# Performance work log

Measured on AMD Instinct MI355X. Metric: run time of the kernel, lower is better.

The kernel has to match this reference:

```python
import jax, jax.numpy as jnp
import numpy as np

EMBED_DIMS = 192
NUM_HEADS = 6
WH, WW = 7, 7
N_TOK = WH * WW
B_WIN = 4096


def _rpe_index(Wh, Ww):
    coords = np.array([[x, y] for x in range(Ww) for y in range(Wh)])  # [N,2]
    d = coords[None, :, :] - coords[:, None, :]                        # [N,N,2]
    idx = (d[:, :, 0] + Ww - 1) * (2 * Ww - 1) + (d[:, :, 1] + Wh - 1)
    return idx.T  # transpose(0,1) as in the torch code


def setup_inputs() -> dict:
    key = jax.random.key(0)
    ks = jax.random.split(key, 6)
    C = EMBED_DIMS
    return {
        "x": jax.random.normal(ks[0], (B_WIN, N_TOK, C), dtype=jnp.float32),
        "qkv_w": jax.random.normal(ks[1], (3 * C, C), dtype=jnp.float32) * 0.02,
        "qkv_b": jax.random.normal(ks[2], (3 * C,), dtype=jnp.float32) * 0.02,
        "proj_w": jax.random.normal(ks[3], (C, C), dtype=jnp.float32) * 0.02,
        "proj_b": jax.random.normal(ks[4], (C,), dtype=jnp.float32) * 0.02,
        "rpe_table": jax.random.normal(ks[5], ((2 * WH - 1) * (2 * WW - 1), NUM_HEADS), dtype=jnp.float32),
        "rpe_idx": jnp.asarray(_rpe_index(WH, WW), dtype=jnp.int32),
    }


def reference(x, qkv_w, qkv_b, proj_w, proj_b, rpe_table, rpe_idx):
    B, N, C = x.shape
    H = NUM_HEADS
    hd = C // H
    scale = hd ** -0.5
    # qkv projection: torch Linear is x @ W.T + b
    qkv = x @ qkv_w.T + qkv_b                      # [B, N, 3C]
    qkv = qkv.reshape(B, N, 3, H, hd).transpose(2, 0, 3, 1, 4)  # [3, B, H, N, hd]
    q, k, v = qkv[0] * scale, qkv[1], qkv[2]
    attn = jnp.einsum("bhnd,bhmd->bhnm", q, k)     # [B, H, N, N]
    # relative position bias gather: table[idx] -> [N, N, H] -> [H, N, N]
    bias = rpe_table[rpe_idx].transpose(2, 0, 1)
    attn = jax.nn.softmax(attn + bias, axis=-1)
    out = jnp.einsum("bhnm,bhmd->bhnd", attn, v)   # [B, H, N, hd]
    out = out.transpose(0, 2, 1, 3).reshape(B, N, C)
    return out @ proj_w.T + proj_b
```

## Files before the change

kernel.cpp:

```cpp
#include <hip/hip_runtime.h>
#include <stdint.h>

#define NWIN 4096
#define NTOK 49
#define CDIM 192
#define NH   6
#define HD   32

typedef __attribute__((ext_vector_type(8))) short short8;
typedef __attribute__((ext_vector_type(4))) float floatx4;
typedef unsigned short ushort_t;
typedef unsigned int uint32;

#define XS_S 200
#define QK_S 136
#define P_S  72
#define VT_S 72

#define OFF_XS   0
#define OFF_QKS  9800
#define OFF_PB   16464
#define OFF_VT   19992
#define LDS_TOT  24600

__device__ __forceinline__ ushort_t f2bf(float f) {
    uint32 u = __float_as_uint(f);
    u += 0x7fffu + ((u >> 16) & 1u);
    return (ushort_t)(u >> 16);
}

__global__ void wmsa_prologue(const float* __restrict__ qkv_w,
                              const float* __restrict__ proj_w,
                              const float* __restrict__ rpe_table,
                              const int*   __restrict__ rpe_idx,
                              ushort_t* __restrict__ qkv_wb,
                              ushort_t* __restrict__ proj_wb,
                              float* __restrict__ biasws)
{
    int i = blockIdx.x * 256 + threadIdx.x;
    if (i < 110592) {
        qkv_wb[i] = f2bf(qkv_w[i]);
    } else if (i < 147456) {
        proj_wb[i - 110592] = f2bf(proj_w[i - 110592]);
    } else if (i < 147456 + NH * NTOK * 64) {
        int r = i - 147456;
        int h = r / (NTOK * 64);
        int rem = r - h * (NTOK * 64);
        int n = rem >> 6, m = rem & 63;
        biasws[r] = (m < NTOK) ? rpe_table[rpe_idx[n * NTOK + m] * NH + h] : 0.f;
    }
}

__global__ __launch_bounds__(256)
void wmsa_mfma(const float* __restrict__ x,
               const ushort_t* __restrict__ qkv_wb,
               const float* __restrict__ qkv_b,
               const ushort_t* __restrict__ proj_wb,
               const float* __restrict__ proj_b,
               const float* __restrict__ biasws,
               float* __restrict__ out)
{
    __shared__ alignas(16) ushort_t lds[LDS_TOT];
    ushort_t* const xs  = lds + OFF_XS;
    ushort_t* const qks = lds + OFF_QKS;
    ushort_t* const Pb  = lds + OFF_PB;
    ushort_t* const Vt  = lds + OFF_VT;

    const int b    = blockIdx.x;
    const int t    = threadIdx.x;
    const int w    = t >> 6;
    const int lane = t & 63;
    const int quad = lane >> 4;
    const int c    = lane & 15;
    const float scale = 0.17677669529663687f;

    const float* xb = x + (size_t)b * (NTOK * CDIM);

    for (int i = t; i < (NTOK * CDIM) / 4; i += 256) {
        int e = i * 4;
        int n = e / CDIM, d = e - n * CDIM;
        float4 v = *(const float4*)(xb + e);
        ushort_t* p = &xs[n * XS_S + d];
        p[0] = f2bf(v.x); p[1] = f2bf(v.y); p[2] = f2bf(v.z); p[3] = f2bf(v.w);
    }
    __syncthreads();

    floatx4 out_acc[NH][2];
    const floatx4 zf = {0.f, 0.f, 0.f, 0.f};
    #pragma unroll
    for (int h = 0; h < NH; ++h) { out_acc[h][0] = zf; out_acc[h][1] = zf; }

    const int hh_w   = w >> 1;
    const int half_w = w & 1;
    const int jcol   = hh_w * 64 + half_w * 16 + c;

    #pragma unroll
    for (int pass = 0; pass < 3; ++pass) {
        const int jbase = (2 * pass + hh_w) * HD + half_w * 16 + c;
        floatx4 acc[3][4];
        #pragma unroll
        for (int s = 0; s < 3; ++s)
            #pragma unroll
            for (int mt = 0; mt < 4; ++mt) acc[s][mt] = zf;

        #pragma unroll
        for (int ks = 0; ks < 6; ++ks) {
            short8 a4[4];
            #pragma unroll
            for (int mt = 0; mt < 4; ++mt)
                a4[mt] = *(const short8*)&xs[(mt * 16 + c) * XS_S + ks * 32 + quad * 8];
            #pragma unroll
            for (int s = 0; s < 3; ++s) {
                short8 bf = *(const short8*)&qkv_wb[(s * CDIM + jbase) * CDIM + ks * 32 + quad * 8];
                #pragma unroll
                for (int mt = 0; mt < 4; ++mt)
                    acc[s][mt] = __builtin_amdgcn_mfma_f32_16x16x32_bf16(
                        a4[mt], bf, acc[s][mt], 0, 0, 0);
            }
        }
        float bq = qkv_b[jbase];
        float bk = qkv_b[CDIM + jbase];
        float bv = qkv_b[2 * CDIM + jbase];
        #pragma unroll
        for (int mt = 0; mt < 4; ++mt) {
            #pragma unroll
            for (int r = 0; r < 4; ++r) {
                int n = mt * 16 + quad * 4 + r;
                if (n < NTOK) {
                    qks[n * QK_S + jcol]      = f2bf((acc[0][mt][r] + bq) * scale);
                    qks[n * QK_S + jcol + 32] = f2bf(acc[1][mt][r] + bk);
                }
                Vt[(w * 16 + c) * VT_S + n] =
                    (n < NTOK) ? f2bf(acc[2][mt][r] + bv) : (ushort_t)0;
            }
        }
        __syncthreads();

        #pragma unroll
        for (int hh = 0; hh < 2; ++hh) {
            const int h = pass * 2 + hh;

            short8 aq = *(const short8*)&qks[(w * 16 + c) * QK_S + hh * 64 + quad * 8];
            floatx4 sacc[4];
            #pragma unroll
            for (int nt = 0; nt < 4; ++nt) {
                short8 bk8 = *(const short8*)&qks[(nt * 16 + c) * QK_S + hh * 64 + 32 + quad * 8];
                sacc[nt] = __builtin_amdgcn_mfma_f32_16x16x32_bf16(aq, bk8, zf, 0, 0, 0);
            }

            const float* bpb = biasws + h * (NTOK * 64);
            #pragma unroll
            for (int r = 0; r < 4; ++r) {
                int n  = w * 16 + quad * 4 + r;
                int nc = (n < NTOK) ? n : (NTOK - 1);
                float sv[4];
                #pragma unroll
                for (int nt = 0; nt < 4; ++nt) {
                    int col = nt * 16 + c;
                    float bias = bpb[nc * 64 + col];
                    sv[nt] = (col < NTOK) ? (sacc[nt][r] + bias) : -1e30f;
                }
                float m0 = fmaxf(fmaxf(sv[0], sv[1]), fmaxf(sv[2], sv[3]));
                m0 = fmaxf(m0, __shfl_xor(m0, 1));
                m0 = fmaxf(m0, __shfl_xor(m0, 2));
                m0 = fmaxf(m0, __shfl_xor(m0, 4));
                m0 = fmaxf(m0, __shfl_xor(m0, 8));
                float ex[4], s0 = 0.f;
                #pragma unroll
                for (int nt = 0; nt < 4; ++nt) { ex[nt] = __expf(sv[nt] - m0); s0 += ex[nt]; }
                s0 += __shfl_xor(s0, 1);
                s0 += __shfl_xor(s0, 2);
                s0 += __shfl_xor(s0, 4);
                s0 += __shfl_xor(s0, 8);
                float inv = 1.f / s0;
                if (n < NTOK) {
                    #pragma unroll
                    for (int nt = 0; nt < 4; ++nt)
                        Pb[n * P_S + nt * 16 + c] = f2bf(ex[nt] * inv);
                }
            }

            #pragma unroll
            for (int ks2 = 0; ks2 < 2; ++ks2) {
                short8 ap = *(const short8*)&Pb[(w * 16 + c) * P_S + ks2 * 32 + quad * 8];
                #pragma unroll
                for (int nt = 0; nt < 2; ++nt) {
                    short8 bv8 = *(const short8*)&Vt[(hh * HD + nt * 16 + c) * VT_S + ks2 * 32 + quad * 8];
                    out_acc[h][nt] = __builtin_amdgcn_mfma_f32_16x16x32_bf16(
                        ap, bv8, out_acc[h][nt], 0, 0, 0);
                }
            }
        }
        if (pass < 2) __syncthreads();
    }

    #pragma unroll
    for (int h = 0; h < NH; ++h)
        #pragma unroll
        for (int nt = 0; nt < 2; ++nt)
            #pragma unroll
            for (int r = 0; r < 4; ++r) {
                int n = w * 16 + quad * 4 + r;
                if (n < NTOK)
                    xs[n * XS_S + h * HD + nt * 16 + c] = f2bf(out_acc[h][nt][r]);
            }
    __syncthreads();

    floatx4 pacc[3][4];
    #pragma unroll
    for (int tt = 0; tt < 3; ++tt)
        #pragma unroll
        for (int mt = 0; mt < 4; ++mt) pacc[tt][mt] = zf;

    #pragma unroll
    for (int ks = 0; ks < 6; ++ks) {
        short8 a4[4];
        #pragma unroll
        for (int mt = 0; mt < 4; ++mt)
            a4[mt] = *(const short8*)&xs[(mt * 16 + c) * XS_S + ks * 32 + quad * 8];
        #pragma unroll
        for (int tt = 0; tt < 3; ++tt) {
            int j = (tt * 4 + w) * 16 + c;
            short8 bf = *(const short8*)&proj_wb[j * CDIM + ks * 32 + quad * 8];
            #pragma unroll
            for (int mt = 0; mt < 4; ++mt)
                pacc[tt][mt] = __builtin_amdgcn_mfma_f32_16x16x32_bf16(
                    a4[mt], bf, pacc[tt][mt], 0, 0, 0);
        }
    }
    #pragma unroll
    for (int tt = 0; tt < 3; ++tt) {
        int j = (tt * 4 + w) * 16 + c;
        float pb = proj_b[j];
        #pragma unroll
        for (int mt = 0; mt < 4; ++mt)
            #pragma unroll
            for (int r = 0; r < 4; ++r) {
                int n = mt * 16 + quad * 4 + r;
                if (n < NTOK)
                    out[((size_t)b * NTOK + n) * CDIM + j] = pacc[tt][mt][r] + pb;
            }
    }
}

extern "C" void kernel_launch(void* const* d_in, const int* in_sizes, int n_in,
                              void* d_out, int out_size, void* d_ws, size_t ws_size,
                              hipStream_t stream)
{
    const float* x      = (const float*)d_in[0];
    const float* qkv_w  = (const float*)d_in[1];
    const float* qkv_b  = (const float*)d_in[2];
    const float* proj_w = (const float*)d_in[3];
    const float* proj_b = (const float*)d_in[4];
    const float* rpe_t  = (const float*)d_in[5];
    const int*   rpe_i  = (const int*)d_in[6];
    float*       o      = (float*)d_out;

    ushort_t* qkv_wb  = (ushort_t*)d_ws;
    ushort_t* proj_wb = qkv_wb + 110592;
    float*    biasws  = (float*)((char*)d_ws + (110592 + 36864) * sizeof(ushort_t));

    int tot = 147456 + NH * NTOK * 64;
    wmsa_prologue<<<dim3((tot + 255) / 256), dim3(256), 0, stream>>>(
        qkv_w, proj_w, rpe_t, rpe_i, qkv_wb, proj_wb, biasws);
    wmsa_mfma<<<dim3(NWIN), dim3(256), 0, stream>>>(
        x, qkv_wb, qkv_b, proj_wb, proj_b, biasws, o);
}
```

Baseline: 593.7 us.

## Repartition MMA work so each wave owns a 16-row token tile

Each wave now owns one 16-token row block across all matmuls instead of splitting output columns across waves. It keeps its x fragments in registers for the whole QKV stage and writes per-head attention outputs straight into LDS, which drops the 48 out_acc accumulators and one barrier. It also adds launch_bounds(256,3) to cut register pressure and raise occupancy. The cost is that each wave now reloads every QKV and projection weight fragment from global memory/L2 on its own, instead of reusing one B fragment across four M tiles, so weight traffic per block grows.

```diff
diff --git a/kernel.cpp b/kernel.cpp
--- a/kernel.cpp
+++ b/kernel.cpp
@@ -51,7 +51,7 @@
     }
 }
 
-__global__ __launch_bounds__(256)
+__global__ __launch_bounds__(256, 3)
 void wmsa_mfma(const float* __restrict__ x,
                const ushort_t* __restrict__ qkv_wb,
                const float* __restrict__ qkv_b,
@@ -73,6 +73,7 @@
     const int quad = lane >> 4;
     const int c    = lane & 15;
     const float scale = 0.17677669529663687f;
+    const floatx4 zf = {0.f, 0.f, 0.f, 0.f};
 
     const float* xb = x + (size_t)b * (NTOK * CDIM);
 
@@ -85,53 +86,48 @@
     }
     __syncthreads();
 
-    floatx4 out_acc[NH][2];
-    const floatx4 zf = {0.f, 0.f, 0.f, 0.f};
+    const int arow = w * 16 + c;
+    short8 af[6];
     #pragma unroll
-    for (int h = 0; h < NH; ++h) { out_acc[h][0] = zf; out_acc[h][1] = zf; }
-
-    const int hh_w   = w >> 1;
-    const int half_w = w & 1;
-    const int jcol   = hh_w * 64 + half_w * 16 + c;
-
-    #pragma unroll
+    for (int ks = 0; ks < 6; ++ks)
+        af[ks] = *(const short8*)&xs[arow * XS_S + ks * 32 + quad * 8];
+
     for (int pass = 0; pass < 3; ++pass) {
-        const int jbase = (2 * pass + hh_w) * HD + half_w * 16 + c;
-        floatx4 acc[3][4];
-        #pragma unroll
-        for (int s = 0; s < 3; ++s)
-            #pragma unroll
-            for (int mt = 0; mt < 4; ++mt) acc[s][mt] = zf;
-
-        #pragma unroll
-        for (int ks = 0; ks < 6; ++ks) {
-            short8 a4[4];
-            #pragma unroll
-            for (int mt = 0; mt < 4; ++mt)
-                a4[mt] = *(const short8*)&xs[(mt * 16 + c) * XS_S + ks * 32 + quad * 8];
-            #pragma unroll
-            for (int s = 0; s < 3; ++s) {
-                short8 bf = *(const short8*)&qkv_wb[(s * CDIM + jbase) * CDIM + ks * 32 + quad * 8];
+        #pragma unroll
+        for (int tg = 0; tg < 4; ++tg) {
+            const int hh   = tg >> 1;
+            const int half = tg & 1;
+            const int jb   = (2 * pass + hh) * HD + half * 16 + c;
+            const ushort_t* wp0 = qkv_wb + jb * CDIM + quad * 8;
+
+            floatx4 acc[3];
+            #pragma unroll
+            for (int s = 0; s < 3; ++s) acc[s] = zf;
+
+            #pragma unroll
+            for (int ks = 0; ks < 6; ++ks) {
                 #pragma unroll
-                for (int mt = 0; mt < 4; ++mt)
-                    acc[s][mt] = __builtin_amdgcn_mfma_f32_16x16x32_bf16(
-                        a4[mt], bf, acc[s][mt], 0, 0, 0);
-            }
-        }
-        float bq = qkv_b[jbase];
-        float bk = qkv_b[CDIM + jbase];
-        float bv = qkv_b[2 * CDIM + jbase];
-        #pragma unroll
-        for (int mt = 0; mt < 4; ++mt) {
-            #pragma unroll
-            for (int r = 0; r < 4; ++r) {
-                int n = mt * 16 + quad * 4 + r;
+                for (int s = 0; s < 3; ++s) {
+                    short8 bf = *(const short8*)(wp0 + s * (CDIM * CDIM) + ks * 32);
+                    acc[s] = __builtin_amdgcn_mfma_f32_16x16x32_bf16(
+                        af[ks], bf, acc[s], 0, 0, 0);
+                }
+            }
+
+            float bq = qkv_b[jb];
+            float bk = qkv_b[CDIM + jb];
+            float bv = qkv_b[2 * CDIM + jb];
+            const int qcol = hh * 64 + half * 16 + c;
+            const int vrow = hh * HD + half * 16 + c;
+            #pragma unroll
+            for (int r = 0; r < 4; ++r) {
+                int n = w * 16 + quad * 4 + r;
                 if (n < NTOK) {
-                    qks[n * QK_S + jcol]      = f2bf((acc[0][mt][r] + bq) * scale);
-                    qks[n * QK_S + jcol + 32] = f2bf(acc[1][mt][r] + bk);
-                }
-                Vt[(w * 16 + c) * VT_S + n] =
-                    (n < NTOK) ? f2bf(acc[2][mt][r] + bv) : (ushort_t)0;
+                    qks[n * QK_S + qcol]      = f2bf((acc[0][r] + bq) * scale);
+                    qks[n * QK_S + qcol + 32] = f2bf(acc[1][r] + bk);
+                }
+                Vt[vrow * VT_S + n] = (n < NTOK) ? f2bf(acc[2][r] + bv)
+                                                 : (ushort_t)0;
             }
         }
         __syncthreads();
@@ -140,7 +136,7 @@
         for (int hh = 0; hh < 2; ++hh) {
             const int h = pass * 2 + hh;
 
-            short8 aq = *(const short8*)&qks[(w * 16 + c) * QK_S + hh * 64 + quad * 8];
+            short8 aq = *(const short8*)&qks[arow * QK_S + hh * 64 + quad * 8];
             floatx4 sacc[4];
             #pragma unroll
             for (int nt = 0; nt < 4; ++nt) {
@@ -180,66 +176,59 @@
                 }
             }
 
+            floatx4 o0 = zf, o1 = zf;
             #pragma unroll
             for (int ks2 = 0; ks2 < 2; ++ks2) {
-                short8 ap = *(const short8*)&Pb[(w * 16 + c) * P_S + ks2 * 32 + quad * 8];
-                #pragma unroll
-                for (int nt = 0; nt < 2; ++nt) {
-                    short8 bv8 = *(const short8*)&Vt[(hh * HD + nt * 16 + c) * VT_S + ks2 * 32 + quad * 8];
-                    out_acc[h][nt] = __builtin_amdgcn_mfma_f32_16x16x32_bf16(
-                        ap, bv8, out_acc[h][nt], 0, 0, 0);
+                short8 ap  = *(const short8*)&Pb[arow * P_S + ks2 * 32 + quad * 8];
+                short8 bv0 = *(const short8*)&Vt[(hh * HD + c) * VT_S + ks2 * 32 + quad * 8];
+                short8 bv1 = *(const short8*)&Vt[(hh * HD + 16 + c) * VT_S + ks2 * 32 + quad * 8];
+                o0 = __builtin_amdgcn_mfma_f32_16x16x32_bf16(ap, bv0, o0, 0, 0, 0);
+                o1 = __builtin_amdgcn_mfma_f32_16x16x32_bf16(ap, bv1, o1, 0, 0, 0);
+            }
+            #pragma unroll
+            for (int r = 0; r < 4; ++r) {
+                int n = w * 16 + quad * 4 + r;
+                if (n < NTOK) {
+                    xs[n * XS_S + h * HD + c]      = f2bf(o0[r]);
+                    xs[n * XS_S + h * HD + 16 + c] = f2bf(o1[r]);
                 }
             }
         }
         if (pass < 2) __syncthreads();
     }
 
+    short8 ap6[6];
     #pragma unroll
-    for (int h = 0; h < NH; ++h)
-        #pragma unroll
-        for (int nt = 0; nt < 2; ++nt)
+    for (int ks = 0; ks < 6; ++ks)
+        ap6[ks] = *(const short8*)&xs[arow * XS_S + ks * 32 + quad * 8];
+
+    #pragma unroll
+    for (int tg = 0; tg < 4; ++tg) {
+        floatx4 pacc[3];
+        #pragma unroll
+        for (int tt = 0; tt < 3; ++tt) pacc[tt] = zf;
+
+        #pragma unroll
+        for (int ks = 0; ks < 6; ++ks) {
+            #pragma unroll
+            for (int tt = 0; tt < 3; ++tt) {
+                int j = (tg * 3 + tt) * 16 + c;
+                short8 bf = *(const short8*)&proj_wb[j * CDIM + ks * 32 + quad * 8];
+                pacc[tt] = __builtin_amdgcn_mfma_f32_16x16x32_bf16(
+                    ap6[ks], bf, pacc[tt], 0, 0, 0);
+            }
+        }
+        #pragma unroll
+        for (int tt = 0; tt < 3; ++tt) {
+            int j = (tg * 3 + tt) * 16 + c;
+            float pb = proj_b[j];
             #pragma unroll
             for (int r = 0; r < 4; ++r) {
                 int n = w * 16 + quad * 4 + r;
                 if (n < NTOK)
-                    xs[n * XS_S + h * HD + nt * 16 + c] = f2bf(out_acc[h][nt][r]);
-            }
-    __syncthreads();
-
-    floatx4 pacc[3][4];
-    #pragma unroll
-    for (int tt = 0; tt < 3; ++tt)
-        #pragma unroll
-        for (int mt = 0; mt < 4; ++mt) pacc[tt][mt] = zf;
-
-    #pragma unroll
-    for (int ks = 0; ks < 6; ++ks) {
-        short8 a4[4];
-        #pragma unroll
-        for (int mt = 0; mt < 4; ++mt)
-            a4[mt] = *(const short8*)&xs[(mt * 16 + c) * XS_S + ks * 32 + quad * 8];
-        #pragma unroll
-        for (int tt = 0; tt < 3; ++tt) {
-            int j = (tt * 4 + w) * 16 + c;
-            short8 bf = *(const short8*)&proj_wb[j * CDIM + ks * 32 + quad * 8];
-            #pragma unroll
-            for (int mt = 0; mt < 4; ++mt)
-                pacc[tt][mt] = __builtin_amdgcn_mfma_f32_16x16x32_bf16(
-                    a4[mt], bf, pacc[tt][mt], 0, 0, 0);
-        }
-    }
-    #pragma unroll
-    for (int tt = 0; tt < 3; ++tt) {
-        int j = (tt * 4 + w) * 16 + c;
-        float pb = proj_b[j];
-        #pragma unroll
-        for (int mt = 0; mt < 4; ++mt)
-            #pragma unroll
-            for (int r = 0; r < 4; ++r) {
-                int n = mt * 16 + quad * 4 + r;
-                if (n < NTOK)
-                    out[((size_t)b * NTOK + n) * CDIM + j] = pacc[tt][mt][r] + pb;
-            }
+                    out[((size_t)b * NTOK + n) * CDIM + j] = pacc[tt][r] + pb;
+            }
+        }
     }
 }
 
```

Result: slower. 940.5 us (+58.4%).

## Pack per-head attention outputs to bf16 registers and raise occupancy bound

Applied to the files above, without the earlier changes.

Replaces the 12 fp32 accumulator vectors held across all passes with per-head temporary accumulators that are packed into bf16 pairs, and writes the first four heads into xs before the last pass once xs is no longer needed. Adds a min-blocks-per-SM hint of 3 to launch_bounds. The aim is to cut register pressure so more workgroups fit per CU. The price is extra packing and unpacking instructions, and possible spills if the compiler is forced under the tighter register limit.

```diff
diff --git a/kernel.cpp b/kernel.cpp
--- a/kernel.cpp
+++ b/kernel.cpp
@@ -27,6 +27,9 @@
     uint32 u = __float_as_uint(f);
     u += 0x7fffu + ((u >> 16) & 1u);
     return (ushort_t)(u >> 16);
+}
+__device__ __forceinline__ uint32 pk2(float lo, float hi) {
+    return (uint32)f2bf(lo) | ((uint32)f2bf(hi) << 16);
 }
 
 __global__ void wmsa_prologue(const float* __restrict__ qkv_w,
@@ -51,7 +54,7 @@
     }
 }
 
-__global__ __launch_bounds__(256)
+__global__ __launch_bounds__(256, 3)
 void wmsa_mfma(const float* __restrict__ x,
                const ushort_t* __restrict__ qkv_wb,
                const float* __restrict__ qkv_b,
@@ -73,6 +76,7 @@
     const int quad = lane >> 4;
     const int c    = lane & 15;
     const float scale = 0.17677669529663687f;
+    const floatx4 zf = {0.f, 0.f, 0.f, 0.f};
 
     const float* xb = x + (size_t)b * (NTOK * CDIM);
 
@@ -85,18 +89,19 @@
     }
     __syncthreads();
 
-    floatx4 out_acc[NH][2];
-    const floatx4 zf = {0.f, 0.f, 0.f, 0.f};
-    #pragma unroll
-    for (int h = 0; h < NH; ++h) { out_acc[h][0] = zf; out_acc[h][1] = zf; }
+    uint32 out_pk[4][2][2];
 
     const int hh_w   = w >> 1;
     const int half_w = w & 1;
     const int jcol   = hh_w * 64 + half_w * 16 + c;
+    const int vrow   = w * 16 + c;
+    const int arow   = w * 16 + c;
 
     #pragma unroll
     for (int pass = 0; pass < 3; ++pass) {
-        const int jbase = (2 * pass + hh_w) * HD + half_w * 16 + c;
+        const int jb = (2 * pass + hh_w) * HD + half_w * 16 + c;
+        const ushort_t* wp0 = qkv_wb + jb * CDIM + quad * 8;
+
         floatx4 acc[3][4];
         #pragma unroll
         for (int s = 0; s < 3; ++s)
@@ -111,16 +116,16 @@
                 a4[mt] = *(const short8*)&xs[(mt * 16 + c) * XS_S + ks * 32 + quad * 8];
             #pragma unroll
             for (int s = 0; s < 3; ++s) {
-                short8 bf = *(const short8*)&qkv_wb[(s * CDIM + jbase) * CDIM + ks * 32 + quad * 8];
+                short8 bf = *(const short8*)(wp0 + s * (CDIM * CDIM) + ks * 32);
                 #pragma unroll
                 for (int mt = 0; mt < 4; ++mt)
                     acc[s][mt] = __builtin_amdgcn_mfma_f32_16x16x32_bf16(
                         a4[mt], bf, acc[s][mt], 0, 0, 0);
             }
         }
-        float bq = qkv_b[jbase];
-        float bk = qkv_b[CDIM + jbase];
-        float bv = qkv_b[2 * CDIM + jbase];
+        float bq = qkv_b[jb];
+        float bk = qkv_b[CDIM + jb];
+        float bv = qkv_b[2 * CDIM + jb];
         #pragma unroll
         for (int mt = 0; mt < 4; ++mt) {
             #pragma unroll
@@ -130,17 +135,33 @@
                     qks[n * QK_S + jcol]      = f2bf((acc[0][mt][r] + bq) * scale);
                     qks[n * QK_S + jcol + 32] = f2bf(acc[1][mt][r] + bk);
                 }
-                Vt[(w * 16 + c) * VT_S + n] =
-                    (n < NTOK) ? f2bf(acc[2][mt][r] + bv) : (ushort_t)0;
+                Vt[vrow * VT_S + n] = (n < NTOK) ? f2bf(acc[2][mt][r] + bv)
+                                                 : (ushort_t)0;
             }
         }
         __syncthreads();
+
+        if (pass == 2) {
+            #pragma unroll
+            for (int h2 = 0; h2 < 4; ++h2)
+                #pragma unroll
+                for (int nt = 0; nt < 2; ++nt)
+                    #pragma unroll
+                    for (int r = 0; r < 4; ++r) {
+                        int n = w * 16 + quad * 4 + r;
+                        if (n < NTOK) {
+                            uint32 d = out_pk[h2][nt][r >> 1];
+                            xs[n * XS_S + h2 * HD + nt * 16 + c] =
+                                (ushort_t)((r & 1) ? (d >> 16) : (d & 0xffffu));
+                        }
+                    }
+        }
 
         #pragma unroll
         for (int hh = 0; hh < 2; ++hh) {
             const int h = pass * 2 + hh;
 
-            short8 aq = *(const short8*)&qks[(w * 16 + c) * QK_S + hh * 64 + quad * 8];
+            short8 aq = *(const short8*)&qks[arow * QK_S + hh * 64 + quad * 8];
             floatx4 sacc[4];
             #pragma unroll
             for (int nt = 0; nt < 4; ++nt) {
@@ -180,31 +201,35 @@
                 }
             }
 
+            floatx4 o2[2]; o2[0] = zf; o2[1] = zf;
             #pragma unroll
             for (int ks2 = 0; ks2 < 2; ++ks2) {
-                short8 ap = *(const short8*)&Pb[(w * 16 + c) * P_S + ks2 * 32 + quad * 8];
+                short8 ap = *(const short8*)&Pb[arow * P_S + ks2 * 32 + quad * 8];
                 #pragma unroll
                 for (int nt = 0; nt < 2; ++nt) {
                     short8 bv8 = *(const short8*)&Vt[(hh * HD + nt * 16 + c) * VT_S + ks2 * 32 + quad * 8];
-                    out_acc[h][nt] = __builtin_amdgcn_mfma_f32_16x16x32_bf16(
-                        ap, bv8, out_acc[h][nt], 0, 0, 0);
-                }
-            }
-        }
-        if (pass < 2) __syncthreads();
-    }
-
-    #pragma unroll
-    for (int h = 0; h < NH; ++h)
-        #pragma unroll
-        for (int nt = 0; nt < 2; ++nt)
-            #pragma unroll
-            for (int r = 0; r < 4; ++r) {
-                int n = w * 16 + quad * 4 + r;
-                if (n < NTOK)
-                    xs[n * XS_S + h * HD + nt * 16 + c] = f2bf(out_acc[h][nt][r]);
-            }
-    __syncthreads();
+                    o2[nt] = __builtin_amdgcn_mfma_f32_16x16x32_bf16(ap, bv8, o2[nt], 0, 0, 0);
+                }
+            }
+            if (pass < 2) {
+                #pragma unroll
+                for (int nt = 0; nt < 2; ++nt) {
+                    out_pk[h][nt][0] = pk2(o2[nt][0], o2[nt][1]);
+                    out_pk[h][nt][1] = pk2(o2[nt][2], o2[nt][3]);
+                }
+            } else {
+                #pragma unroll
+                for (int nt = 0; nt < 2; ++nt)
+                    #pragma unroll
+                    for (int r = 0; r < 4; ++r) {
+                        int n = w * 16 + quad * 4 + r;
+                        if (n < NTOK)
+                            xs[n * XS_S + h * HD + nt * 16 + c] = f2bf(o2[nt][r]);
+                    }
+            }
+        }
+        __syncthreads();
+    }
 
     floatx4 pacc[3][4];
     #pragma unroll
```

Result: faster. 504.9 us (-15.0%).
